# Kernel tuning notes

Measured on AMD Instinct MI355X. Metric: run time of the kernel, lower is better.

The kernel has to match this reference:

```python
import jax, jax.numpy as jnp
import numpy as np

N_NODES = 50000
N_EDGES = 800000
IN_DIM = 128
HID_DIM = 64
OUT_DIM = 40
N_REL = 8


def setup_inputs() -> dict:
    key = jax.random.key(0)
    ks = jax.random.split(key, 12)
    x = jax.random.normal(ks[0], (N_NODES, IN_DIM), dtype=jnp.float32)
    edge_index = jax.random.randint(ks[1], (2, N_EDGES), 0, N_NODES, dtype=jnp.int64)
    edge_type = jax.random.randint(ks[2], (N_EDGES,), 0, N_REL, dtype=jnp.int64)
    s = 0.05
    W1 = jax.random.normal(ks[3], (N_REL, IN_DIM, HID_DIM), dtype=jnp.float32) * s
    root1 = jax.random.normal(ks[4], (IN_DIM, HID_DIM), dtype=jnp.float32) * s
    b1 = jnp.zeros((HID_DIM,), dtype=jnp.float32)
    W2 = jax.random.normal(ks[5], (N_REL, HID_DIM, HID_DIM), dtype=jnp.float32) * s
    root2 = jax.random.normal(ks[6], (HID_DIM, HID_DIM), dtype=jnp.float32) * s
    b2 = jnp.zeros((HID_DIM,), dtype=jnp.float32)
    Wl = jax.random.normal(ks[7], (HID_DIM, OUT_DIM), dtype=jnp.float32) * s
    bl = jnp.zeros((OUT_DIM,), dtype=jnp.float32)
    return {"x": x, "edge_index": edge_index, "edge_type": edge_type,
            "W1": W1, "root1": root1, "b1": b1,
            "W2": W2, "root2": root2, "b2": b2,
            "Wl": Wl, "bl": bl}


def _rgcn_conv(x, W, Wroot, b, src, dst, edge_type):
    # PyG RGCNConv (no bases/blocks, aggr='mean'):
    #   out[i] = sum_r mean_{(j->i) of rel r} (x[j] @ W[r]) + x[i] @ Wroot + b
    N = x.shape[0]
    R = W.shape[0]
    h = jnp.einsum('ni,rio->rno', x, W)        # [R, N, out]
    msgs = h[edge_type, src]                   # [E, out] edge gather
    seg = edge_type * N + dst                  # per (relation, dst) segment
    sums = jax.ops.segment_sum(msgs, seg, num_segments=R * N)
    cnt = jax.ops.segment_sum(jnp.ones((msgs.shape[0],), x.dtype), seg,
                              num_segments=R * N)
    mean = sums / jnp.maximum(cnt, 1.0)[:, None]
    agg = mean.reshape(R, N, -1).sum(axis=0)   # sum over relations
    return agg + x @ Wroot + b


def reference(x, edge_index, edge_type, W1, root1, b1, W2, root2, b2, Wl, bl):
    src, dst = edge_index[0], edge_index[1]
    h = jax.nn.relu(_rgcn_conv(x, W1, root1, b1, src, dst, edge_type))
    # dropout is identity in eval mode
    h = jax.nn.relu(_rgcn_conv(h, W2, root2, b2, src, dst, edge_type))
    logits = h @ Wl + bl
    return jax.nn.log_softmax(logits, axis=1)
```

## Files before the change

### kernel.cpp

```cpp
#include <hip/hip_runtime.h>
#include <hip/hip_bf16.h>
#include <cmath>

#define IN_DIM 128
#define HID 64
#define OUT_DIM 40
#define NREL 8
#define NCOLS 576
#define CAP 64
#define CSTR 16

typedef __attribute__((ext_vector_type(8))) short short8;
typedef __attribute__((ext_vector_type(4))) short short4v;
typedef __attribute__((ext_vector_type(4))) float floatx4;
typedef __attribute__((ext_vector_type(2))) float f32x2;

static __device__ __forceinline__ short f2bf(float f) {
  __hip_bfloat16 h = __float2bfloat16(f);
  return __builtin_bit_cast(short, h);
}
static __device__ __forceinline__ float bflo(unsigned int u) {
  return __int_as_float(u << 16);
}
static __device__ __forceinline__ float bfhi(unsigned int u) {
  return __int_as_float(u & 0xffff0000u);
}
static __device__ __forceinline__ unsigned int packbf(float x, float y) {
  unsigned int lo = (unsigned short)f2bf(x);
  unsigned int hi = (unsigned short)f2bf(y);
  return lo | (hi << 16);
}

__global__ void pack_bt(const float* __restrict__ W1, const float* __restrict__ root1,
                        short* __restrict__ Bt1,
                        const float* __restrict__ W2, const float* __restrict__ root2,
                        short* __restrict__ Bt2) {
  const int PB1 = (NCOLS * IN_DIM + 255) / 256;
  int b = blockIdx.x;
  if (b < PB1) {
    int i = b * 256 + threadIdx.x;
    if (i >= NCOLS * IN_DIM) return;
    int c = i / IN_DIM, k = i % IN_DIM;
    float v = (c < NREL * HID)
      ? W1[((size_t)(c >> 6) * IN_DIM + k) * HID + (c & 63)]
      : root1[(size_t)k * HID + (c - NREL * HID)];
    Bt1[i] = f2bf(v);
  } else {
    int i = (b - PB1) * 256 + threadIdx.x;
    if (i >= NCOLS * HID) return;
    int c = i / HID, k = i % HID;
    float v = (c < NREL * HID)
      ? W2[((size_t)(c >> 6) * HID + k) * HID + (c & 63)]
      : root2[(size_t)k * HID + (c - NREL * HID)];
    Bt2[i] = f2bf(v);
  }
}

template<int K, int AMODE>
__device__ __forceinline__ void gemm_dev(
    short* As, short* Bs,
    const void* __restrict__ Aptr, const short* __restrict__ Bt,
    const float* __restrict__ bias, short* __restrict__ H,
    unsigned short* __restrict__ AGG, int M, int row0)
{
  constexpr int AST = K + 8;
  int tid = threadIdx.x;
  int wv = tid >> 6, lane = tid & 63;
  int lm = lane & 15, quad = lane >> 4;

  if (AMODE == 0) {
    const float* A = (const float*)Aptr;
    constexpr int CH = K / 4;
    for (int i = tid; i < 64 * CH; i += 256) {
      int r = i / CH, kq = i % CH;
      int gr = row0 + r; if (gr >= M) gr = M - 1;
      float4 v = *(const float4*)(A + (unsigned)(gr * K + kq * 4));
      short4v s;
      s.x = f2bf(v.x); s.y = f2bf(v.y); s.z = f2bf(v.z); s.w = f2bf(v.w);
      *(short4v*)(As + r * AST + kq * 4) = s;
    }
  } else {
    const short* A = (const short*)Aptr;
    constexpr int CH = K / 8;
    for (int i = tid; i < 64 * CH; i += 256) {
      int r = i / CH, ko = i % CH;
      int gr = row0 + r; if (gr >= M) gr = M - 1;
      short8 v = *(const short8*)(A + (unsigned)(gr * K + ko * 8));
      #pragma unroll
      for (int j = 0; j < 8; ++j)
        if ((unsigned short)v[j] & 0x8000u) v[j] = 0;
      *(short8*)(As + r * AST + ko * 8) = v;
    }
  }

  const short* ap = As + (16 * wv + lm) * AST + quad * 8;

  for (int cy = 0; cy < 9; ++cy) {
    constexpr int CB = K / 8;
    for (int i = tid; i < 64 * CB; i += 256) {
      int n = i / CB, ko = i % CB;
      short8 v = *(const short8*)(Bt + (unsigned)((cy * 64 + n) * K + ko * 8));
      *(short8*)(Bs + n * AST + ko * 8) = v;
    }
    __syncthreads();

    floatx4 acc[4] = {{0,0,0,0},{0,0,0,0},{0,0,0,0},{0,0,0,0}};
    #pragma unroll
    for (int ks = 0; ks < K / 32; ++ks) {
      short8 a = *(const short8*)(ap + ks * 32);
      #pragma unroll
      for (int nb = 0; nb < 4; ++nb) {
        short8 b = *(const short8*)(Bs + (nb * 16 + lm) * AST + ks * 32 + quad * 8);
        acc[nb] = __builtin_amdgcn_mfma_f32_16x16x32_bf16(a, b, acc[nb], 0, 0, 0);
      }
    }
    __syncthreads();

    int mbase = row0 + 16 * wv + quad * 4;
    if (cy < 8) {
      #pragma unroll
      for (int nb = 0; nb < 4; ++nb) {
        int col = cy * 64 + nb * 16 + lm;
        #pragma unroll
        for (int r = 0; r < 4; ++r) {
          int mg = mbase + r;
          if (mg < M) H[(unsigned)mg * (NREL * HID) + col] = f2bf(acc[nb][r]);
        }
      }
    } else {
      #pragma unroll
      for (int nb = 0; nb < 4; ++nb) {
        int col = nb * 16 + lm;
        float bv = bias[col];
        #pragma unroll
        for (int r = 0; r < 4; ++r) {
          int mg = mbase + r;
          if (mg < M)
            AGG[(unsigned)mg * HID + col] = (unsigned short)f2bf(acc[nb][r] + bv);
        }
      }
    }
  }
}

__global__ __launch_bounds__(256, 4) void gemm1_scatter(
    const float* __restrict__ A, const short* __restrict__ Bt,
    const float* __restrict__ bias, short* __restrict__ H,
    unsigned short* __restrict__ AGG, int M, int GB,
    const int* __restrict__ src, const int* __restrict__ dst,
    const int* __restrict__ et,
    int* __restrict__ cursor, int* __restrict__ ev, int E)
{
  constexpr int AST = IN_DIM + 8;
  __shared__ short As[64 * AST];
  __shared__ short Bs[64 * AST];
  if ((int)blockIdx.x < GB) {
    gemm_dev<IN_DIM, 0>(As, Bs, A, Bt, bias, H, AGG, M, blockIdx.x * 64);
  } else {
    int e = (blockIdx.x - GB) * 256 + threadIdx.x;
    if (e >= E) return;
    int d = dst[e];
    int pos = atomicAdd(&cursor[d * CSTR], 1);
    if (pos < CAP)
      __builtin_nontemporal_store((src[e] << 3) | et[e], &ev[d * CAP + pos]);
  }
}

__global__ __launch_bounds__(256, 4) void gemm2_mfma(
    const unsigned short* __restrict__ A, const short* __restrict__ Bt,
    const float* __restrict__ bias, short* __restrict__ H,
    unsigned short* __restrict__ AGG, int M)
{
  constexpr int AST = HID + 8;
  __shared__ short As[64 * AST];
  __shared__ short Bs[64 * AST];
  gemm_dev<HID, 1>(As, Bs, A, Bt, bias, H, AGG, M, blockIdx.x * 64);
}

__global__ __launch_bounds__(256) void csr_agg_fe(
    const short* __restrict__ H, const int* __restrict__ cursor,
    int* __restrict__ ev, unsigned short* __restrict__ AGG, int N)
{
  int d = blockIdx.x * 4 + (threadIdx.x >> 6);
  if (d >= N) return;
  int lane = threadIdx.x & 63;
  int q = lane >> 4, sub = lane & 15;
  int cnt = cursor[d * CSTR]; if (cnt > CAP) cnt = CAP;
  int* evrow = ev + d * CAP;

  int ew = (lane < cnt) ? evrow[lane] : 0;
  int t = ew & 7;
  int code = 64;
  float wt = 0.f;
  #pragma unroll
  for (int r = 0; r < 8; ++r) {
    unsigned long long m = __ballot(lane < cnt && t == r);
    int c = __popcll(m);
    if (lane < cnt && t == r) { code = c - 1; wt = 1.0f / (float)(c > 0 ? c : 1); }
  }
  evrow[lane] = (ew << 7) | code;

  float a0, a1, a2, a3;
  uint2* aggrow = (uint2*)(AGG + (size_t)d * HID);
  uint2 iv = aggrow[sub];
  a0 = (q == 0) ? bflo(iv.x) : 0.f;
  a1 = (q == 0) ? bfhi(iv.x) : 0.f;
  a2 = (q == 0) ? bflo(iv.y) : 0.f;
  a3 = (q == 0) ? bfhi(iv.y) : 0.f;

  const uint2* Hu2 = (const uint2*)H;
  f32x2 A01 = {a0, a1}, A23 = {a2, a3};
  int npass = (cnt + 31) >> 5;
  for (int P = 0; P < npass; ++P) {
    int base = P * 32 + q * 8;
    int ee[8]; float ww[8];
    #pragma unroll
    for (int i = 0; i < 8; ++i) {
      int j = base + i;
      int jj = j < cnt ? j : cnt - 1;
      ee[i] = __shfl(ew, jj, 64);
      float w = __shfl(wt, jj, 64);
      ww[i] = (j < cnt) ? w : 0.f;
    }
    uint2 hv[8];
    #pragma unroll
    for (int i = 0; i < 8; ++i)
      hv[i] = Hu2[(unsigned)ee[i] * 16u + (unsigned)sub];
    #pragma unroll
    for (int i = 0; i < 8; ++i) {
      f32x2 w2 = {ww[i], ww[i]};
      f32x2 h01 = {bflo(hv[i].x), bfhi(hv[i].x)};
      f32x2 h23 = {bflo(hv[i].y), bfhi(hv[i].y)};
      A01 += h01 * w2;
      A23 += h23 * w2;
    }
  }
  a0 = A01.x; a1 = A01.y; a2 = A23.x; a3 = A23.y;
  a0 += __shfl_xor(a0, 16, 64); a0 += __shfl_xor(a0, 32, 64);
  a1 += __shfl_xor(a1, 16, 64); a1 += __shfl_xor(a1, 32, 64);
  a2 += __shfl_xor(a2, 16, 64); a2 += __shfl_xor(a2, 32, 64);
  a3 += __shfl_xor(a3, 16, 64); a3 += __shfl_xor(a3, 32, 64);

  if (q == 0) {
    uint2 ov;
    ov.x = packbf(a0, a1);
    ov.y = packbf(a2, a3);
    aggrow[sub] = ov;
  }
}

static __device__ __forceinline__ void agg_fast(
    const uint2* __restrict__ Hu2, const int* __restrict__ evrow,
    int npass, int q, int sub, const float* __restrict__ lut,
    float& a0, float& a1, float& a2, float& a3)
{
  f32x2 A01 = {a0, a1}, A23 = {a2, a3};
  for (int P = 0; P < npass; ++P) {
    const int4* pp = (const int4*)(evrow + P * 32 + q * 8);
    int4 v0 = pp[0], v1 = pp[1];
    int vv[8] = {v0.x, v0.y, v0.z, v0.w, v1.x, v1.y, v1.z, v1.w};
    uint2 hv[8];
    float ww[8];
    #pragma unroll
    for (int i = 0; i < 8; ++i) {
      hv[i] = Hu2[(unsigned)(vv[i] >> 7) * 16u + (unsigned)sub];
      ww[i] = lut[vv[i] & 127];
    }
    #pragma unroll
    for (int i = 0; i < 8; ++i) {
      f32x2 w2 = {ww[i], ww[i]};
      f32x2 h01 = {bflo(hv[i].x), bfhi(hv[i].x)};
      f32x2 h23 = {bflo(hv[i].y), bfhi(hv[i].y)};
      A01 += h01 * w2;
      A23 += h23 * w2;
    }
  }
  a0 = A01.x; a1 = A01.y; a2 = A23.x; a3 = A23.y;
  a0 += __shfl_xor(a0, 16, 64); a0 += __shfl_xor(a0, 32, 64);
  a1 += __shfl_xor(a1, 16, 64); a1 += __shfl_xor(a1, 32, 64);
  a2 += __shfl_xor(a2, 16, 64); a2 += __shfl_xor(a2, 32, 64);
  a3 += __shfl_xor(a3, 16, 64); a3 += __shfl_xor(a3, 32, 64);
}

__global__ __launch_bounds__(256) void csr_agg_final(
    const short* __restrict__ H, const int* __restrict__ cursor,
    const int* __restrict__ ev, const unsigned short* __restrict__ AGG,
    const float* __restrict__ Wl, const float* __restrict__ bl,
    float* __restrict__ out, int N)
{
  __shared__ float sWl[HID * OUT_DIM];
  __shared__ float sbl[OUT_DIM];
  __shared__ float sh[4][HID];
  __shared__ float lut[128];
  int tid = threadIdx.x;
  int wv = tid >> 6, lane = tid & 63;
  int q = lane >> 4, sub = lane & 15;
  int d = blockIdx.x * 4 + wv;
  bool valid = d < N;
  int dc = valid ? d : (N - 1);

  int cnt = cursor[dc * CSTR]; if (cnt > CAP) cnt = CAP;
  uint2 iv = ((const uint2*)(AGG + (size_t)dc * HID))[sub];

  for (int i = tid; i < HID * OUT_DIM; i += 256) sWl[i] = Wl[i];
  if (tid < OUT_DIM) sbl[tid] = bl[tid];
  if (tid < 128) lut[tid] = (tid < 64) ? 1.0f / (float)(tid + 1) : 0.f;
  __syncthreads();

  float a0 = 0.f, a1 = 0.f, a2 = 0.f, a3 = 0.f;
  if (q == 0) {
    a0 = bflo(iv.x); a1 = bfhi(iv.x); a2 = bflo(iv.y); a3 = bfhi(iv.y);
  }
  int npass = (cnt + 31) >> 5;
  if (npass > 0)
    agg_fast((const uint2*)H, ev + dc * CAP, npass, q, sub, lut, a0, a1, a2, a3);
  if (q == 0) {
    float4 v;
    v.x = fmaxf(a0, 0.f); v.y = fmaxf(a1, 0.f);
    v.z = fmaxf(a2, 0.f); v.w = fmaxf(a3, 0.f);
    *(float4*)(&sh[wv][4 * sub]) = v;
  }
  __syncthreads();

  float logit = -__builtin_inff();
  if (lane < OUT_DIM) {
    float t = sbl[lane];
    #pragma unroll 8
    for (int k = 0; k < HID; ++k) t += sh[wv][k] * sWl[k * OUT_DIM + lane];
    logit = t;
  }
  float m = logit;
  #pragma unroll
  for (int o = 32; o > 0; o >>= 1) m = fmaxf(m, __shfl_xor(m, o, 64));
  float ex = (lane < OUT_DIM) ? expf(logit - m) : 0.f;
  float s = ex;
  #pragma unroll
  for (int o = 32; o > 0; o >>= 1) s += __shfl_xor(s, o, 64);
  if (valid && lane < OUT_DIM)
    out[(size_t)d * OUT_DIM + lane] = logit - m - logf(s);
}

extern "C" void kernel_launch(void* const* d_in, const int* in_sizes, int n_in,
                              void* d_out, int out_size, void* d_ws, size_t ws_size,
                              hipStream_t stream) {
  const float* x     = (const float*)d_in[0];
  const int*   eidx  = (const int*)d_in[1];
  const int*   etype = (const int*)d_in[2];
  const float* W1    = (const float*)d_in[3];
  const float* root1 = (const float*)d_in[4];
  const float* b1    = (const float*)d_in[5];
  const float* W2    = (const float*)d_in[6];
  const float* root2 = (const float*)d_in[7];
  const float* b2    = (const float*)d_in[8];
  const float* Wl    = (const float*)d_in[9];
  const float* bl    = (const float*)d_in[10];

  int N = in_sizes[0] / IN_DIM;
  int E = in_sizes[2];
  const int* srcp = eidx;
  const int* dstp = eidx + E;

  char* ws = (char*)d_ws;
  size_t off = 0;
  auto alloc = [&](size_t bytes) -> char* {
    char* p = ws + off;
    off += (bytes + 255) & ~(size_t)255;
    return p;
  };
  short* Bt1    = (short*)alloc((size_t)NCOLS * IN_DIM * 2);
  short* Bt2    = (short*)alloc((size_t)NCOLS * HID * 2);
  int*   cursor = (int*)alloc((size_t)N * CSTR * 4);
  int*   ev     = (int*)alloc((size_t)N * CAP * 4);
  short* H1     = (short*)alloc((size_t)N * NREL * HID * 2);
  short* H2     = (short*)alloc((size_t)N * NREL * HID * 2);
  unsigned short* AGG1 = (unsigned short*)alloc((size_t)N * HID * 2);
  unsigned short* AGG2 = (unsigned short*)alloc((size_t)N * HID * 2);

  hipMemsetAsync(cursor, 0, (size_t)N * CSTR * 4, stream);

  const int PB1 = (NCOLS * IN_DIM + 255) / 256;
  const int PB2 = (NCOLS * HID + 255) / 256;
  pack_bt<<<PB1 + PB2, 256, 0, stream>>>(W1, root1, Bt1, W2, root2, Bt2);

  int GB = (N + 63) / 64;
  int SB = (E + 255) / 256;
  gemm1_scatter<<<GB + SB, 256, 0, stream>>>(x, Bt1, b1, H1, AGG1, N, GB,
                                             srcp, dstp, etype, cursor, ev, E);

  csr_agg_fe<<<(N + 3) / 4, 256, 0, stream>>>(H1, cursor, ev, AGG1, N);

  gemm2_mfma<<<GB, 256, 0, stream>>>(AGG1, Bt2, b2, H2, AGG2, N);

  csr_agg_final<<<(N + 3) / 4, 256, 0, stream>>>(H2, cursor, ev, AGG2,
                                                 Wl, bl, (float*)d_out, N);
}
```

Measured before the change: 232.8 us.

## Split edge finalization into own kernel and aggregate two nodes per wavefront

```diff
diff --git a/kernel.cpp b/kernel.cpp
--- a/kernel.cpp
+++ b/kernel.cpp
@@ -177,55 +177,42 @@
   gemm_dev<HID, 1>(As, Bs, A, Bt, bias, H, AGG, M, blockIdx.x * 64);
 }
 
-__global__ __launch_bounds__(256) void csr_agg_fe(
-    const short* __restrict__ H, const int* __restrict__ cursor,
-    int* __restrict__ ev, unsigned short* __restrict__ AGG, int N)
+__global__ __launch_bounds__(256) void finalize_ev(
+    const int* __restrict__ cursor, int* __restrict__ ev, int N)
 {
   int d = blockIdx.x * 4 + (threadIdx.x >> 6);
   if (d >= N) return;
   int lane = threadIdx.x & 63;
-  int q = lane >> 4, sub = lane & 15;
   int cnt = cursor[d * CSTR]; if (cnt > CAP) cnt = CAP;
-  int* evrow = ev + d * CAP;
-
-  int ew = (lane < cnt) ? evrow[lane] : 0;
-  int t = ew & 7;
+  int e = (lane < cnt) ? ev[d * CAP + lane] : 0;
+  int t = e & 7;
   int code = 64;
-  float wt = 0.f;
   #pragma unroll
   for (int r = 0; r < 8; ++r) {
     unsigned long long m = __ballot(lane < cnt && t == r);
     int c = __popcll(m);
-    if (lane < cnt && t == r) { code = c - 1; wt = 1.0f / (float)(c > 0 ? c : 1); }
-  }
-  evrow[lane] = (ew << 7) | code;
-
-  float a0, a1, a2, a3;
-  uint2* aggrow = (uint2*)(AGG + (size_t)d * HID);
-  uint2 iv = aggrow[sub];
-  a0 = (q == 0) ? bflo(iv.x) : 0.f;
-  a1 = (q == 0) ? bfhi(iv.x) : 0.f;
-  a2 = (q == 0) ? bflo(iv.y) : 0.f;
-  a3 = (q == 0) ? bfhi(iv.y) : 0.f;
-
-  const uint2* Hu2 = (const uint2*)H;
+    if (lane < cnt && t == r) code = c - 1;
+  }
+  ev[d * CAP + lane] = (lane < cnt) ? ((e << 7) | code) : 64;
+}
+
+static __device__ __forceinline__ void agg_half(
+    const uint2* __restrict__ Hu2, const int* __restrict__ evrow,
+    int npass, int qloc, int sub, const float* __restrict__ lut,
+    float& a0, float& a1, float& a2, float& a3)
+{
   f32x2 A01 = {a0, a1}, A23 = {a2, a3};
-  int npass = (cnt + 31) >> 5;
   for (int P = 0; P < npass; ++P) {
-    int base = P * 32 + q * 8;
-    int ee[8]; float ww[8];
+    const int4* pp = (const int4*)(evrow + P * 16 + qloc * 8);
+    int4 v0 = pp[0], v1 = pp[1];
+    int vv[8] = {v0.x, v0.y, v0.z, v0.w, v1.x, v1.y, v1.z, v1.w};
+    uint2 hv[8];
+    float ww[8];
     #pragma unroll
     for (int i = 0; i < 8; ++i) {
-      int j = base + i;
-      int jj = j < cnt ? j : cnt - 1;
-      ee[i] = __shfl(ew, jj, 64);
-      float w = __shfl(wt, jj, 64);
-      ww[i] = (j < cnt) ? w : 0.f;
-    }
-    uint2 hv[8];
-    #pragma unroll
-    for (int i = 0; i < 8; ++i)
-      hv[i] = Hu2[(unsigned)ee[i] * 16u + (unsigned)sub];
+      hv[i] = Hu2[(unsigned)(vv[i] >> 7) * 16u + (unsigned)sub];
+      ww[i] = lut[vv[i] & 127];
+    }
     #pragma unroll
     for (int i = 0; i < 8; ++i) {
       f32x2 w2 = {ww[i], ww[i]};
@@ -236,50 +223,42 @@
     }
   }
   a0 = A01.x; a1 = A01.y; a2 = A23.x; a3 = A23.y;
-  a0 += __shfl_xor(a0, 16, 64); a0 += __shfl_xor(a0, 32, 64);
-  a1 += __shfl_xor(a1, 16, 64); a1 += __shfl_xor(a1, 32, 64);
-  a2 += __shfl_xor(a2, 16, 64); a2 += __shfl_xor(a2, 32, 64);
-  a3 += __shfl_xor(a3, 16, 64); a3 += __shfl_xor(a3, 32, 64);
-
-  if (q == 0) {
+  a0 += __shfl_xor(a0, 16, 64);
+  a1 += __shfl_xor(a1, 16, 64);
+  a2 += __shfl_xor(a2, 16, 64);
+  a3 += __shfl_xor(a3, 16, 64);
+}
+
+__global__ __launch_bounds__(256) void csr_agg(
+    const short* __restrict__ H, const int* __restrict__ cursor,
+    const int* __restrict__ ev, unsigned short* __restrict__ AGG, int N)
+{
+  __shared__ float lut[128];
+  int tid = threadIdx.x;
+  if (tid < 128) lut[tid] = (tid < 64) ? 1.0f / (float)(tid + 1) : 0.f;
+  __syncthreads();
+
+  int wv = tid >> 6, lane = tid & 63;
+  int h = lane >> 5, lhl = lane & 31, qloc = lhl >> 4, sub = lhl & 15;
+  int d = blockIdx.x * 8 + wv * 2 + h;
+  if (d >= N) return;
+
+  int cnt = cursor[d * CSTR]; if (cnt > CAP) cnt = CAP;
+  float a0 = 0.f, a1 = 0.f, a2 = 0.f, a3 = 0.f;
+  uint2* aggrow = (uint2*)(AGG + (size_t)d * HID);
+  if (qloc == 0) {
+    uint2 iv = aggrow[sub];
+    a0 = bflo(iv.x); a1 = bfhi(iv.x); a2 = bflo(iv.y); a3 = bfhi(iv.y);
+  }
+  int npass = (cnt + 15) >> 4;
+  if (npass > 0)
+    agg_half((const uint2*)H, ev + d * CAP, npass, qloc, sub, lut, a0, a1, a2, a3);
+  if (qloc == 0) {
     uint2 ov;
     ov.x = packbf(a0, a1);
     ov.y = packbf(a2, a3);
     aggrow[sub] = ov;
   }
-}
-
-static __device__ __forceinline__ void agg_fast(
-    const uint2* __restrict__ Hu2, const int* __restrict__ evrow,
-    int npass, int q, int sub, const float* __restrict__ lut,
-    float& a0, float& a1, float& a2, float& a3)
-{
-  f32x2 A01 = {a0, a1}, A23 = {a2, a3};
-  for (int P = 0; P < npass; ++P) {
-    const int4* pp = (const int4*)(evrow + P * 32 + q * 8);
-    int4 v0 = pp[0], v1 = pp[1];
-    int vv[8] = {v0.x, v0.y, v0.z, v0.w, v1.x, v1.y, v1.z, v1.w};
-    uint2 hv[8];
-    float ww[8];
-    #pragma unroll
-    for (int i = 0; i < 8; ++i) {
-      hv[i] = Hu2[(unsigned)(vv[i] >> 7) * 16u + (unsigned)sub];
-      ww[i] = lut[vv[i] & 127];
-    }
-    #pragma unroll
-    for (int i = 0; i < 8; ++i) {
-      f32x2 w2 = {ww[i], ww[i]};
-      f32x2 h01 = {bflo(hv[i].x), bfhi(hv[i].x)};
-      f32x2 h23 = {bflo(hv[i].y), bfhi(hv[i].y)};
-      A01 += h01 * w2;
-      A23 += h23 * w2;
-    }
-  }
-  a0 = A01.x; a1 = A01.y; a2 = A23.x; a3 = A23.y;
-  a0 += __shfl_xor(a0, 16, 64); a0 += __shfl_xor(a0, 32, 64);
-  a1 += __shfl_xor(a1, 16, 64); a1 += __shfl_xor(a1, 32, 64);
-  a2 += __shfl_xor(a2, 16, 64); a2 += __shfl_xor(a2, 32, 64);
-  a3 += __shfl_xor(a3, 16, 64); a3 += __shfl_xor(a3, 32, 64);
 }
 
 __global__ __launch_bounds__(256) void csr_agg_final(
@@ -290,14 +269,13 @@
 {
   __shared__ float sWl[HID * OUT_DIM];
   __shared__ float sbl[OUT_DIM];
-  __shared__ float sh[4][HID];
+  __shared__ float sh[8][HID];
   __shared__ float lut[128];
   int tid = threadIdx.x;
   int wv = tid >> 6, lane = tid & 63;
-  int q = lane >> 4, sub = lane & 15;
-  int d = blockIdx.x * 4 + wv;
-  bool valid = d < N;
-  int dc = valid ? d : (N - 1);
+  int h = lane >> 5, lhl = lane & 31, qloc = lhl >> 4, sub = lhl & 15;
+  int d = blockIdx.x * 8 + wv * 2 + h;
+  int dc = d < N ? d : N - 1;
 
   int cnt = cursor[dc * CSTR]; if (cnt > CAP) cnt = CAP;
   uint2 iv = ((const uint2*)(AGG + (size_t)dc * HID))[sub];
@@ -308,36 +286,41 @@
   __syncthreads();
 
   float a0 = 0.f, a1 = 0.f, a2 = 0.f, a3 = 0.f;
-  if (q == 0) {
+  if (qloc == 0) {
     a0 = bflo(iv.x); a1 = bfhi(iv.x); a2 = bflo(iv.y); a3 = bfhi(iv.y);
   }
-  int npass = (cnt + 31) >> 5;
+  int npass = (cnt + 15) >> 4;
   if (npass > 0)
-    agg_fast((const uint2*)H, ev + dc * CAP, npass, q, sub, lut, a0, a1, a2, a3);
-  if (q == 0) {
+    agg_half((const uint2*)H, ev + dc * CAP, npass, qloc, sub, lut, a0, a1, a2, a3);
+  if (qloc == 0) {
     float4 v;
     v.x = fmaxf(a0, 0.f); v.y = fmaxf(a1, 0.f);
     v.z = fmaxf(a2, 0.f); v.w = fmaxf(a3, 0.f);
-    *(float4*)(&sh[wv][4 * sub]) = v;
+    *(float4*)(&sh[wv * 2 + h][4 * sub]) = v;
   }
   __syncthreads();
 
-  float logit = -__builtin_inff();
-  if (lane < OUT_DIM) {
-    float t = sbl[lane];
-    #pragma unroll 8
-    for (int k = 0; k < HID; ++k) t += sh[wv][k] * sWl[k * OUT_DIM + lane];
-    logit = t;
-  }
-  float m = logit;
   #pragma unroll
-  for (int o = 32; o > 0; o >>= 1) m = fmaxf(m, __shfl_xor(m, o, 64));
-  float ex = (lane < OUT_DIM) ? expf(logit - m) : 0.f;
-  float s = ex;
-  #pragma unroll
-  for (int o = 32; o > 0; o >>= 1) s += __shfl_xor(s, o, 64);
-  if (valid && lane < OUT_DIM)
-    out[(size_t)d * OUT_DIM + lane] = logit - m - logf(s);
+  for (int ii = 0; ii < 2; ++ii) {
+    int dd = blockIdx.x * 8 + wv * 2 + ii;
+    const float* row = sh[wv * 2 + ii];
+    float logit = -__builtin_inff();
+    if (lane < OUT_DIM) {
+      float t = sbl[lane];
+      #pragma unroll 8
+      for (int k = 0; k < HID; ++k) t += row[k] * sWl[k * OUT_DIM + lane];
+      logit = t;
+    }
+    float m = logit;
+    #pragma unroll
+    for (int o = 32; o > 0; o >>= 1) m = fmaxf(m, __shfl_xor(m, o, 64));
+    float ex = (lane < OUT_DIM) ? expf(logit - m) : 0.f;
+    float s = ex;
+    #pragma unroll
+    for (int o = 32; o > 0; o >>= 1) s += __shfl_xor(s, o, 64);
+    if (dd < N && lane < OUT_DIM)
+      out[(size_t)dd * OUT_DIM + lane] = logit - m - logf(s);
+  }
 }
 
 extern "C" void kernel_launch(void* const* d_in, const int* in_sizes, int n_in,
@@ -387,10 +370,12 @@
   gemm1_scatter<<<GB + SB, 256, 0, stream>>>(x, Bt1, b1, H1, AGG1, N, GB,
                                              srcp, dstp, etype, cursor, ev, E);
 
-  csr_agg_fe<<<(N + 3) / 4, 256, 0, stream>>>(H1, cursor, ev, AGG1, N);
+  finalize_ev<<<(N + 3) / 4, 256, 0, stream>>>(cursor, ev, N);
+
+  csr_agg<<<(N + 7) / 8, 256, 0, stream>>>(H1, cursor, ev, AGG1, N);
 
   gemm2_mfma<<<GB, 256, 0, stream>>>(AGG1, Bt2, b2, H2, AGG2, N);
 
-  csr_agg_final<<<(N + 3) / 4, 256, 0, stream>>>(H2, cursor, ev, AGG2,
+  csr_agg_final<<<(N + 7) / 8, 256, 0, stream>>>(H2, cursor, ev, AGG2,
                                                  Wl, bl, (float*)d_out, N);
 }
```

Result: faster. 227.1 us (-2.5%).
